# Optimization experiments

Measured on AMD Instinct MI355X. Metric: run time of the kernel, lower is better.

## Reference

```python
import jax, jax.numpy as jnp
import numpy as np

B, C, D = 8192, 5994, 192
M, S = 0.2, 30.0
S_NEG = 1.0
COS_M = float(np.cos(M)); SIN_M = float(np.sin(M))
TH = float(np.cos(M))
MM = float(np.sin(np.pi - M) * M)


def _normalize(v):
    # torch F.normalize: v / max(||v||, eps)
    return v / jnp.maximum(jnp.linalg.norm(v, axis=-1, keepdims=True), 1e-12)


def _ce_label_smooth(logits, targets, eps=0.1):
    # torch CrossEntropyLoss(label_smoothing=eps): target dist = (1-eps)*onehot + eps/C
    logp = jax.nn.log_softmax(logits, axis=-1)
    nll = -jnp.take_along_axis(logp, targets[:, None], axis=-1)[:, 0]
    smooth = -logp.mean(axis=-1)
    return ((1.0 - eps) * nll + eps * smooth).mean()


def setup_inputs() -> dict:
    key = jax.random.key(0)
    kx, kw, kl = jax.random.split(key, 3)
    x = jax.random.normal(kx, (B, D), dtype=jnp.float32)
    std = float(np.sqrt(2.0 / (C + D)))  # xavier_normal_ gain=1
    weight = jax.random.normal(kw, (C, D), dtype=jnp.float32) * std
    # guarantee every class appears so n_unique == C (static shapes)
    extra = jax.random.randint(kl, (B - C,), 0, C, dtype=jnp.int32)
    label = jnp.concatenate([jnp.arange(C, dtype=jnp.int32), extra])
    return {"x": x, "weight": weight, "label": label}


def reference(x, weight, label):
    x1 = _normalize(x)           # [B, D]; x2 = x1.clone() in torch => identical values
    w = _normalize(weight)       # [C, D]
    cosine = x1 @ w.T            # [B, C]

    # per-unique-label mean (segment mean); labels_center == arange(C)
    counts = jax.ops.segment_sum(jnp.ones((x1.shape[0],), x1.dtype), label, num_segments=C)
    mean_x = jax.ops.segment_sum(x1, label, num_segments=C) / counts[:, None]  # [C, D]
    cosine_center = mean_x @ w.T  # [C, C]

    # ArcFace margin on centers
    sine_c = jnp.sqrt(jnp.clip(1.0 - cosine_center * cosine_center, 0.0, 1.0))
    phi_c = jnp.where(cosine_center - TH > 0,
                      cosine_center - MM,
                      cosine_center * COS_M - sine_c * SIN_M)
    eye = jnp.eye(C, dtype=cosine_center.dtype)  # one_hot_center with labels arange(C)
    output_center = (eye * phi_c + (1.0 - eye) * cosine_center) * S

    # ArcFace margin on samples
    sine = jnp.sqrt(jnp.clip(1.0 - cosine * cosine, 0.0, 1.0))
    phi = jnp.where(cosine - TH > 0, cosine - MM, cosine * COS_M - sine * SIN_M)
    one_hot = jax.nn.one_hot(label, C, dtype=cosine.dtype)
    output_sample = (one_hot * phi + (1.0 - one_hot) * cosine) * S

    aam_sample_loss = 0.5 * _ce_label_smooth(output_sample, label)
    aam_center_loss = 0.5 * _ce_label_smooth(output_center, jnp.arange(C, dtype=jnp.int32))

    # contrastive term over class means of cat(x1, x2) (x2 == x1)
    logit_neg = jnp.concatenate([mean_x, mean_x], axis=1)  # [C, 2D]
    G = logit_neg @ logit_neg.T                            # [C, C]
    offdiag = ~jnp.eye(C, dtype=bool)                      # torch zeroes diag then filters != 0
    neg_inf = jnp.array(-jnp.inf, G.dtype)
    vmax = jnp.max(jnp.where(offdiag, G, neg_inf))
    lse1 = jax.scipy.special.logsumexp(jnp.where(offdiag, S_NEG * G, neg_inf))
    lse2 = jax.scipy.special.logsumexp(jnp.where(offdiag, (2.0 - vmax) * (1.0 - G / vmax), neg_inf))
    logit_neg_loss = jax.nn.softplus(lse1 - lse2 + vmax)

    loss = logit_neg_loss + aam_center_loss + aam_sample_loss
    # full_unique_index == label here (unique labels are 0..C-1 sorted)
    return loss, output_sample, output_center[label]
```

## Files before the change

kernel.cpp:

```cpp
#include <hip/hip_runtime.h>
#include <cstdint>
#include <cstddef>

#define CCLS 5994
#define CPAD 6016
#define BATCH 8192
#define KDIM 192
#define EMAX 16
#define NCB 47
#define NT0 3008
#define NT1 2209
#define NTG 1128
#define MEGA_NT (NT0 + NT1 + NTG)
#define CEF 32

#define S_SC 30.0f
#define COSM 0.9800665778412416f
#define SINM 0.19866933079506122f
#define THC  0.9800665778412416f
#define MMC  0.039733866159012244f

typedef __attribute__((ext_vector_type(8))) short short8;
typedef __attribute__((ext_vector_type(4))) float f32x4;
typedef __attribute__((ext_vector_type(2))) float f32x2;
typedef unsigned short u16;
typedef unsigned int u32;

__device__ __forceinline__ u16 f2bf(float f) {
  u32 u = __float_as_uint(f);
  u32 r = (u + 0x7FFFu + ((u >> 16) & 1u)) >> 16;
  return (u16)r;
}

__device__ __forceinline__ float bf2f(u16 v) { return __uint_as_float(((u32)v) << 16); }

__device__ __forceinline__ float arc_phi(float c) {
  float s2 = fminf(fmaxf(1.0f - c * c, 0.0f), 1.0f);
  float sine = sqrtf(s2);
  return (c - THC > 0.0f) ? (c - MMC) : (c * COSM - sine * SINM);
}

__device__ __forceinline__ float shift_of(float vmax) {
  return (2.0f - vmax) * (1.0f + 2.0f / vmax);
}

__device__ __forceinline__ float wave_sum(float v) {
#pragma unroll
  for (int off = 1; off < 64; off <<= 1) v += __shfl_xor(v, off);
  return v;
}

__device__ __forceinline__ void tri_decode(int g, int& by, int& bx) {
  by = 0;
  while (g >= NCB - by) { g -= NCB - by; ++by; }
  bx = by + g;
}

__global__ void zero_k(f32x4* __restrict__ p, int n4) {
  const int i = blockIdx.x * 256 + threadIdx.x;
  if (i < n4) p[i] = (f32x4){0.f, 0.f, 0.f, 0.f};
}

__global__ void norm_w_k(const float* __restrict__ w, u16* __restrict__ wb) {
  const int row = blockIdx.x * 4 + (threadIdx.x >> 6);
  const int lane = threadIdx.x & 63;
  float v0 = 0.f, v1 = 0.f, v2 = 0.f;
  if (row < CCLS) {
    const float* p = w + (size_t)row * KDIM;
    v0 = p[lane]; v1 = p[lane + 64]; v2 = p[lane + 128];
  }
  float ss = wave_sum(v0 * v0 + v1 * v1 + v2 * v2);
  float inv = 1.0f / fmaxf(sqrtf(ss), 1e-12f);
  if (row >= CCLS) inv = 0.f;
  u16* q = wb + (size_t)row * KDIM;
  q[lane] = f2bf(v0 * inv);
  q[lane + 64] = f2bf(v1 * inv);
  q[lane + 128] = f2bf(v2 * inv);
}

__global__ void norm_x_k(const float* __restrict__ x, const int* __restrict__ label,
                         u16* __restrict__ xb, int* __restrict__ ecnt, int* __restrict__ eidx,
                         int* __restrict__ dcnt, int* __restrict__ didx) {
  const int row = blockIdx.x * 4 + (threadIdx.x >> 6);
  const int lane = threadIdx.x & 63;
  const float* p = x + (size_t)row * KDIM;
  float v0 = p[lane], v1 = p[lane + 64], v2 = p[lane + 128];
  float ss = wave_sum(v0 * v0 + v1 * v1 + v2 * v2);
  float inv = 1.0f / fmaxf(sqrtf(ss), 1e-12f);
  u16* q = xb + (size_t)row * KDIM;
  q[lane] = f2bf(v0 * inv); q[lane + 64] = f2bf(v1 * inv); q[lane + 128] = f2bf(v2 * inv);
  if (lane == 0) {
    const int lab = label[row];
    int pos = atomicAdd(&ecnt[lab], 1);
    if (pos < EMAX) eidx[lab * EMAX + pos] = row;
    if (row >= CCLS) {
      int dp = atomicAdd(&dcnt[lab], 1);
      if (dp < EMAX) didx[lab * EMAX + dp] = row;
    }
  }
}

__global__ void mean_k(const u16* __restrict__ xb, const int* __restrict__ ecnt,
                       const int* __restrict__ eidx, u16* __restrict__ mb) {
  const int row = blockIdx.x * 4 + (threadIdx.x >> 6);
  const int lane = threadIdx.x & 63;
  u16* q = mb + (size_t)row * KDIM;
  if (row < CCLS) {
    const int n = min(ecnt[row], EMAX);
    float s0 = 0.f, s1 = 0.f, s2 = 0.f;
    for (int j = 0; j < n; ++j) {
      const u16* p = xb + (size_t)eidx[row * EMAX + j] * KDIM;
      s0 += bf2f(p[lane]); s1 += bf2f(p[lane + 64]); s2 += bf2f(p[lane + 128]);
    }
    const float inv = 1.0f / (float)n;
    q[lane] = f2bf(s0 * inv); q[lane + 64] = f2bf(s1 * inv); q[lane + 128] = f2bf(s2 * inv);
  } else {
    q[lane] = 0; q[lane + 64] = 0; q[lane + 128] = 0;
  }
}

__device__ __forceinline__ void stage64(const u16* __restrict__ A, const u16* __restrict__ Bm,
                                        int row0, int col0, int wid, int lane, int k0,
                                        u16* As, u16* Bs) {
  const int sw = (((lane & 7) ^ ((lane >> 3) & 7))) * 8;
#pragma unroll
  for (int i = 0; i < 4; ++i) {
    const int c = wid * 4 + i;
    const int r = c * 8 + (lane >> 3);
    const u16* ga = A + (size_t)(row0 + r) * KDIM + (k0 + sw);
    const u16* gb = Bm + (size_t)(col0 + r) * KDIM + (k0 + sw);
    __builtin_amdgcn_global_load_lds((const __attribute__((address_space(1))) void*)ga,
                                     (__attribute__((address_space(3))) void*)(As + c * 512),
                                     16, 0, 0);
    __builtin_amdgcn_global_load_lds((const __attribute__((address_space(1))) void*)gb,
                                     (__attribute__((address_space(3))) void*)(Bs + c * 512),
                                     16, 0, 0);
  }
}

__device__ __forceinline__ void gemm_core(const u16* __restrict__ A, const u16* __restrict__ Bm,
                                          int row0, int col0, int wid, int lane,
                                          int wm, int wn, u16 (*lds)[8192], f32x4 (&acc)[4][4]) {
#pragma unroll
  for (int i = 0; i < 4; ++i)
#pragma unroll
    for (int j = 0; j < 4; ++j)
      acc[i][j] = (f32x4){0.f, 0.f, 0.f, 0.f};
  for (int k0 = 0; k0 < KDIM; k0 += 64) {
    stage64(A, Bm, row0, col0, wid, lane, k0, &lds[0][0], &lds[1][0]);
    asm volatile("s_waitcnt vmcnt(0)" ::: "memory");
    __syncthreads();
#pragma unroll
    for (int kk = 0; kk < 2; ++kk) {
      short8 af[4], bf[4];
#pragma unroll
      for (int mi = 0; mi < 4; ++mi) {
        const int R = wm * 64 + mi * 16 + (lane & 15);
        const int sl = ((kk * 4 + (lane >> 4)) ^ (lane & 7)) * 8;
        af[mi] = *(const short8*)&lds[0][R * 64 + sl];
      }
#pragma unroll
      for (int ni = 0; ni < 4; ++ni) {
        const int R = wn * 64 + ni * 16 + (lane & 15);
        const int sl = ((kk * 4 + (lane >> 4)) ^ (lane & 7)) * 8;
        bf[ni] = *(const short8*)&lds[1][R * 64 + sl];
      }
#pragma unroll
      for (int mi = 0; mi < 4; ++mi)
#pragma unroll
        for (int ni = 0; ni < 4; ++ni)
          acc[mi][ni] = __builtin_amdgcn_mfma_f32_16x16x32_bf16(af[mi], bf[ni], acc[mi][ni], 0, 0, 0);
    }
    __syncthreads();
  }
}

__device__ __forceinline__ void epi_af(f32x4 (&acc)[4][4], float* __restrict__ out,
                                       const int* __restrict__ label, int is_center, int plane,
                                       int row0, int col0, int bx, int tid, int lane, int wid,
                                       int wm, int wn, u16 (*lds)[8192],
                                       float* __restrict__ pse, float* __restrict__ psm,
                                       float* __restrict__ rowtgt,
                                       const int* __restrict__ dcnt, const int* __restrict__ didx) {
  float* sred = (float*)&lds[0][0];
  const int rl = (lane >> 4) * 4;
  const int cl = lane & 15;
#pragma unroll
  for (int mi = 0; mi < 4; ++mi) {
#pragma unroll
    for (int r = 0; r < 4; ++r) {
      const int gr = row0 + wm * 64 + mi * 16 + rl + r;
      const int valid_r = !is_center || gr < CCLS;
      const int tgt = is_center ? gr : label[gr];
      float se = 0.f, sm = 0.f;
#pragma unroll
      for (int ni = 0; ni < 4; ++ni) {
        const int gc = col0 + wn * 64 + ni * 16 + cl;
        float v = acc[mi][ni][r];
        float val = ((gc == tgt) ? arc_phi(v) : v) * S_SC;
        acc[mi][ni][r] = val;
        if (gc < CCLS && valid_r) {
          se += __expf(val - 30.0f);
          sm += val;
          if (gc == tgt) rowtgt[gr] = val;
        }
      }
#pragma unroll
      for (int m = 1; m < 16; m <<= 1) {
        se += __shfl_xor(se, m);
        sm += __shfl_xor(sm, m);
      }
      if (cl == 0) {
        const int lr = wm * 64 + mi * 16 + rl + r;
        sred[lr * 2 + wn] = se;
        sred[256 + lr * 2 + wn] = sm;
      }
    }
  }
  __syncthreads();
  if (tid < 128) {
    const int gr = row0 + tid;
    if (!is_center || gr < CCLS) {
      float se = sred[tid * 2] + sred[tid * 2 + 1];
      float sm = sred[256 + tid * 2] + sred[256 + tid * 2 + 1];
      pse[(size_t)bx * plane + gr] = se;
      psm[(size_t)bx * plane + gr] = sm;
    }
  }
  float* sC = (float*)&lds[0][0];
#pragma unroll
  for (int half = 0; half < 2; ++half) {
    __syncthreads();
    if (wm == half) {
#pragma unroll
      for (int mi = 0; mi < 4; ++mi)
#pragma unroll
        for (int ni = 0; ni < 4; ++ni)
#pragma unroll
          for (int r = 0; r < 4; ++r)
            sC[(mi * 16 + rl + r) * 128 + wn * 64 + ni * 16 + cl] = acc[mi][ni][r];
    }
    __syncthreads();
#pragma unroll
    for (int i = 0; i < 16; ++i) {
      const int lr = wid * 16 + i;
      const int gr = row0 + half * 64 + lr;
      if (is_center && gr >= CCLS) continue;
      const int gc = col0 + lane * 2;
      if (gc < CCLS) {
        f32x2 v = *(const f32x2*)&sC[lr * 128 + lane * 2];
        __builtin_nontemporal_store(v, (f32x2*)(out + (size_t)gr * CCLS + gc));
      }
    }
    if (is_center) {
      for (int i = 0; i < 16; ++i) {
        const int lr = wid * 16 + i;
        const int gr = row0 + half * 64 + lr;
        if (gr >= CCLS) continue;
        const int n = min(dcnt[gr], EMAX);
        for (int j = 0; j < n; ++j) {
          const int b = didx[gr * EMAX + j];
          const int gc = col0 + lane * 2;
          if (gc < CCLS) {
            f32x2 v = *(const f32x2*)&sC[lr * 128 + lane * 2];
            __builtin_nontemporal_store(v, (f32x2*)(out + (size_t)b * CCLS + gc));
          }
        }
      }
    }
  }
}

__device__ __forceinline__ void epi_gram(f32x4 (&acc)[4][4], float* __restrict__ scal, int pass2,
                                         float aco, float cco, int row0, int col0, int diag,
                                         int tid, int lane, int wid, int wm, int wn,
                                         u16 (*lds)[8192]) {
  float* sred = (float*)&lds[0][0];
  const int rl = (lane >> 4) * 4;
  const int cl = lane & 15;
  float lsum = 0.f;
  float lmax = -3.0e38f;
#pragma unroll
  for (int mi = 0; mi < 4; ++mi)
#pragma unroll
    for (int r = 0; r < 4; ++r) {
      const int gi = row0 + wm * 64 + mi * 16 + rl + r;
#pragma unroll
      for (int ni = 0; ni < 4; ++ni) {
        const int gj = col0 + wn * 64 + ni * 16 + cl;
        if (gi < CCLS && gj < CCLS && gi != gj) {
          float g = 2.0f * acc[mi][ni][r];
          if (!pass2) {
            lsum += __expf(g - 2.0f);
            lmax = fmaxf(lmax, g);
          } else {
            lsum += __expf(fmaf(aco, g, cco));
          }
        }
      }
    }
  const float wgt = diag ? 1.0f : 2.0f;
  lsum = wave_sum(lsum) * wgt;
  if (!pass2) {
#pragma unroll
    for (int off = 1; off < 64; off <<= 1) lmax = fmaxf(lmax, __shfl_xor(lmax, off));
  }
  __syncthreads();
  if (lane == 0) { sred[wid] = lsum; sred[4 + wid] = lmax; }
  __syncthreads();
  if (tid == 0) {
    float s = sred[0] + sred[1] + sred[2] + sred[3];
    atomicAdd(&scal[pass2 ? 2 : 1], s);
    if (!pass2) {
      float m = fmaxf(fmaxf(sred[4], sred[5]), fmaxf(sred[6], sred[7]));
      u32 b = __float_as_uint(m);
      u32 enc = (b & 0x80000000u) ? ~b : (b | 0x80000000u);
      atomicMax((u32*)&scal[0], enc);
    }
  }
}

__launch_bounds__(256)
__global__ void mega_k(const u16* __restrict__ xb, const u16* __restrict__ wb,
                       const u16* __restrict__ mb, const int* __restrict__ label,
                       float* __restrict__ out1, float* __restrict__ out2,
                       float* __restrict__ scal,
                       float* __restrict__ pse_s, float* __restrict__ psm_s,
                       float* __restrict__ rowtgt_s,
                       float* __restrict__ pse_c, float* __restrict__ psm_c,
                       float* __restrict__ rowtgt_c,
                       const int* __restrict__ dcnt, const int* __restrict__ didx) {
  __shared__ u16 lds[2][8192];
  const int tid = threadIdx.x;
  const int lane = tid & 63;
  const int wid = tid >> 6;
  const int wm = wid >> 1, wn = wid & 1;
  const int t = blockIdx.x;

  f32x4 acc[4][4];
  if (t < NT0) {
    const int bx = t % NCB, by = t / NCB;
    gemm_core(xb, wb, by * 128, bx * 128, wid, lane, wm, wn, lds, acc);
    epi_af(acc, out1, label, 0, BATCH, by * 128, bx * 128, bx, tid, lane, wid, wm, wn,
           lds, pse_s, psm_s, rowtgt_s, nullptr, nullptr);
  } else if (t < NT0 + NT1) {
    const int u = t - NT0;
    const int bx = u % NCB, by = u / NCB;
    gemm_core(mb, wb, by * 128, bx * 128, wid, lane, wm, wn, lds, acc);
    epi_af(acc, out2, label, 1, CPAD, by * 128, bx * 128, bx, tid, lane, wid, wm, wn,
           lds, pse_c, psm_c, rowtgt_c, dcnt, didx);
  } else {
    int by, bx;
    tri_decode(t - NT0 - NT1, by, bx);
    gemm_core(mb, mb, by * 128, bx * 128, wid, lane, wm, wn, lds, acc);
    epi_gram(acc, scal, 0, 0.f, 0.f, by * 128, bx * 128, bx == by, tid, lane, wid, wm, wn, lds);
  }
}

__launch_bounds__(256)
__global__ void fin2_k(const u16* __restrict__ mb, float* __restrict__ scal,
                       const float* __restrict__ pse_s, const float* __restrict__ psm_s,
                       const float* __restrict__ rowtgt_s,
                       const float* __restrict__ pse_c, const float* __restrict__ psm_c,
                       const float* __restrict__ rowtgt_c) {
  __shared__ u16 lds[2][8192];
  const int tid = threadIdx.x;
  const int lane = tid & 63;
  const int wid = tid >> 6;
  const int wm = wid >> 1, wn = wid & 1;
  const int t = blockIdx.x;

  if (t < NTG) {
    u32 u = __float_as_uint(scal[0]);
    u32 bits = (u & 0x80000000u) ? (u ^ 0x80000000u) : ~u;
    const float vmax = __uint_as_float(bits);
    const float aco = -(2.0f - vmax) / vmax;
    const float cco = (2.0f - vmax) - shift_of(vmax);
    int by, bx;
    tri_decode(t, by, bx);
    f32x4 acc[4][4];
    gemm_core(mb, mb, by * 128, bx * 128, wid, lane, wm, wn, lds, acc);
    epi_gram(acc, scal, 1, aco, cco, by * 128, bx * 128, bx == by, tid, lane, wid, wm, wn, lds);
  } else {
    const int i = (t - NTG) * 256 + tid;
    float ls = 0.f, lc = 0.f;
    if (i < BATCH) {
      float se = 0.f, sm = 0.f;
#pragma unroll 1
      for (int p = 0; p < NCB; ++p) { se += pse_s[p * BATCH + i]; sm += psm_s[p * BATCH + i]; }
      ls = 30.0f + logf(se) - 0.9f * rowtgt_s[i] - (0.1f / (float)CCLS) * sm;
    }
    if (i < CCLS) {
      float se = 0.f, sm = 0.f;
#pragma unroll 1
      for (int p = 0; p < NCB; ++p) { se += pse_c[p * CPAD + i]; sm += psm_c[p * CPAD + i]; }
      lc = 30.0f + logf(se) - 0.9f * rowtgt_c[i] - (0.1f / (float)CCLS) * sm;
    }
    ls = wave_sum(ls);
    lc = wave_sum(lc);
    if (lane == 0) {
      atomicAdd(&scal[3], ls);
      atomicAdd(&scal[4], lc);
    }
  }
}

__global__ void finalize_k(const float* __restrict__ scal, float* __restrict__ out) {
  u32 u = __float_as_uint(scal[0]);
  u32 bits = (u & 0x80000000u) ? (u ^ 0x80000000u) : ~u;
  float vmax = __uint_as_float(bits);
  float s1 = scal[1], s2 = scal[2], ces = scal[3], cec = scal[4];
  float lse1 = 2.0f + logf(s1);
  float lse2 = shift_of(vmax) + logf(s2);
  float z = lse1 - lse2 + vmax;
  float sp = (z > 20.f) ? z : log1pf(expf(z));
  out[0] = sp + 0.5f * (cec / (float)CCLS) + 0.5f * (ces / (float)BATCH);
}

extern "C" void kernel_launch(void* const* d_in, const int* in_sizes, int n_in,
                              void* d_out, int out_size, void* d_ws, size_t ws_size,
                              hipStream_t stream) {
  (void)in_sizes; (void)n_in; (void)out_size; (void)ws_size;
  const float* x = (const float*)d_in[0];
  const float* w = (const float*)d_in[1];
  const int* label = (const int*)d_in[2];
  float* out = (float*)d_out;
  float* out1 = out + 1;
  float* out2 = out + 1 + (size_t)BATCH * CCLS;

  char* ws = (char*)d_ws;
  size_t o = 0;
  u16* xb = (u16*)(ws + o); o += (size_t)BATCH * KDIM * 2;
  u16* wb = (u16*)(ws + o); o += (size_t)CPAD * KDIM * 2;
  u16* mb = (u16*)(ws + o); o += (size_t)CPAD * KDIM * 2;
  const size_t zo = o;
  float* scal = (float*)(ws + o); o += 256;
  int* ecnt = (int*)(ws + o); o += (size_t)CPAD * 4;
  int* dcnt = (int*)(ws + o); o += (size_t)CPAD * 4;
  const size_t ze = o;
  int* eidx = (int*)(ws + o); o += (size_t)CPAD * EMAX * 4;
  int* didx = (int*)(ws + o); o += (size_t)CPAD * EMAX * 4;
  float* rowtgt_s = (float*)(ws + o); o += (size_t)BATCH * 4;
  float* rowtgt_c = (float*)(ws + o); o += (size_t)CPAD * 4;
  float* pse_s = (float*)(ws + o); o += (size_t)NCB * BATCH * 4;
  float* psm_s = (float*)(ws + o); o += (size_t)NCB * BATCH * 4;
  float* pse_c = (float*)(ws + o); o += (size_t)NCB * CPAD * 4;
  float* psm_c = (float*)(ws + o); o += (size_t)NCB * CPAD * 4;

  const int n4 = (int)((ze - zo) / 16);
  zero_k<<<(n4 + 255) / 256, 256, 0, stream>>>((f32x4*)(ws + zo), n4);

  norm_w_k<<<CPAD / 4, 256, 0, stream>>>(w, wb);
  norm_x_k<<<BATCH / 4, 256, 0, stream>>>(x, label, xb, ecnt, eidx, dcnt, didx);
  mean_k<<<CPAD / 4, 256, 0, stream>>>(xb, ecnt, eidx, mb);

  mega_k<<<MEGA_NT, 256, 0, stream>>>(xb, wb, mb, label, out1, out2, scal,
                                      pse_s, psm_s, rowtgt_s, pse_c, psm_c, rowtgt_c,
                                      dcnt, didx);
  fin2_k<<<NTG + CEF, 256, 0, stream>>>(mb, scal, pse_s, psm_s, rowtgt_s,
                                        pse_c, psm_c, rowtgt_c);

  finalize_k<<<1, 1, 0, stream>>>(scal, out);
}
```

Measured before the change: 291.3 us.

## Replace tiled GEMM-epilogue with per-row-strip blocks that finish CE loss in-block

The 128x128 tiled sample/center GEMM blocks are replaced by 444 strip blocks. Each block owns 32 rows and loops over all 47 column tiles, loading operands straight from global memory without LDS staging. Row-wise softmax sums and the target logit are kept in LDS across the column loop, so each block computes its cross-entropy contribution directly. This removes the per-tile partial-sum buffers and the separate reduction blocks in the second kernel. The trade-off is far fewer blocks, which may underfill the GPU and serialize the large output writes, plus repeated global loads of the weight tile per strip.

```diff
diff --git a/kernel.cpp b/kernel.cpp
--- a/kernel.cpp
+++ b/kernel.cpp
@@ -8,11 +8,11 @@
 #define KDIM 192
 #define EMAX 16
 #define NCB 47
-#define NT0 3008
-#define NT1 2209
+#define NSS 256
+#define NSC 188
+#define NSTRIP (NSS + NSC)
 #define NTG 1128
-#define MEGA_NT (NT0 + NT1 + NTG)
-#define CEF 32
+#define MEGA_NT (NSTRIP + NTG)
 
 #define S_SC 30.0f
 #define COSM 0.9800665778412416f
@@ -175,102 +175,6 @@
   }
 }
 
-__device__ __forceinline__ void epi_af(f32x4 (&acc)[4][4], float* __restrict__ out,
-                                       const int* __restrict__ label, int is_center, int plane,
-                                       int row0, int col0, int bx, int tid, int lane, int wid,
-                                       int wm, int wn, u16 (*lds)[8192],
-                                       float* __restrict__ pse, float* __restrict__ psm,
-                                       float* __restrict__ rowtgt,
-                                       const int* __restrict__ dcnt, const int* __restrict__ didx) {
-  float* sred = (float*)&lds[0][0];
-  const int rl = (lane >> 4) * 4;
-  const int cl = lane & 15;
-#pragma unroll
-  for (int mi = 0; mi < 4; ++mi) {
-#pragma unroll
-    for (int r = 0; r < 4; ++r) {
-      const int gr = row0 + wm * 64 + mi * 16 + rl + r;
-      const int valid_r = !is_center || gr < CCLS;
-      const int tgt = is_center ? gr : label[gr];
-      float se = 0.f, sm = 0.f;
-#pragma unroll
-      for (int ni = 0; ni < 4; ++ni) {
-        const int gc = col0 + wn * 64 + ni * 16 + cl;
-        float v = acc[mi][ni][r];
-        float val = ((gc == tgt) ? arc_phi(v) : v) * S_SC;
-        acc[mi][ni][r] = val;
-        if (gc < CCLS && valid_r) {
-          se += __expf(val - 30.0f);
-          sm += val;
-          if (gc == tgt) rowtgt[gr] = val;
-        }
-      }
-#pragma unroll
-      for (int m = 1; m < 16; m <<= 1) {
-        se += __shfl_xor(se, m);
-        sm += __shfl_xor(sm, m);
-      }
-      if (cl == 0) {
-        const int lr = wm * 64 + mi * 16 + rl + r;
-        sred[lr * 2 + wn] = se;
-        sred[256 + lr * 2 + wn] = sm;
-      }
-    }
-  }
-  __syncthreads();
-  if (tid < 128) {
-    const int gr = row0 + tid;
-    if (!is_center || gr < CCLS) {
-      float se = sred[tid * 2] + sred[tid * 2 + 1];
-      float sm = sred[256 + tid * 2] + sred[256 + tid * 2 + 1];
-      pse[(size_t)bx * plane + gr] = se;
-      psm[(size_t)bx * plane + gr] = sm;
-    }
-  }
-  float* sC = (float*)&lds[0][0];
-#pragma unroll
-  for (int half = 0; half < 2; ++half) {
-    __syncthreads();
-    if (wm == half) {
-#pragma unroll
-      for (int mi = 0; mi < 4; ++mi)
-#pragma unroll
-        for (int ni = 0; ni < 4; ++ni)
-#pragma unroll
-          for (int r = 0; r < 4; ++r)
-            sC[(mi * 16 + rl + r) * 128 + wn * 64 + ni * 16 + cl] = acc[mi][ni][r];
-    }
-    __syncthreads();
-#pragma unroll
-    for (int i = 0; i < 16; ++i) {
-      const int lr = wid * 16 + i;
-      const int gr = row0 + half * 64 + lr;
-      if (is_center && gr >= CCLS) continue;
-      const int gc = col0 + lane * 2;
-      if (gc < CCLS) {
-        f32x2 v = *(const f32x2*)&sC[lr * 128 + lane * 2];
-        __builtin_nontemporal_store(v, (f32x2*)(out + (size_t)gr * CCLS + gc));
-      }
-    }
-    if (is_center) {
-      for (int i = 0; i < 16; ++i) {
-        const int lr = wid * 16 + i;
-        const int gr = row0 + half * 64 + lr;
-        if (gr >= CCLS) continue;
-        const int n = min(dcnt[gr], EMAX);
-        for (int j = 0; j < n; ++j) {
-          const int b = didx[gr * EMAX + j];
-          const int gc = col0 + lane * 2;
-          if (gc < CCLS) {
-            f32x2 v = *(const f32x2*)&sC[lr * 128 + lane * 2];
-            __builtin_nontemporal_store(v, (f32x2*)(out + (size_t)b * CCLS + gc));
-          }
-        }
-      }
-    }
-  }
-}
-
 __device__ __forceinline__ void epi_gram(f32x4 (&acc)[4][4], float* __restrict__ scal, int pass2,
                                          float aco, float cco, int row0, int col0, int diag,
                                          int tid, int lane, int wid, int wm, int wn,
@@ -325,84 +229,171 @@
                        const u16* __restrict__ mb, const int* __restrict__ label,
                        float* __restrict__ out1, float* __restrict__ out2,
                        float* __restrict__ scal,
-                       float* __restrict__ pse_s, float* __restrict__ psm_s,
-                       float* __restrict__ rowtgt_s,
-                       float* __restrict__ pse_c, float* __restrict__ psm_c,
-                       float* __restrict__ rowtgt_c,
                        const int* __restrict__ dcnt, const int* __restrict__ didx) {
+  __shared__ char smem[32768];
+  const int tid = threadIdx.x;
+  const int lane = tid & 63;
+  const int w = tid >> 6;
+  const int t = blockIdx.x;
+
+  if (t < NSTRIP) {
+    float* sC = (float*)smem;
+    float* s_se = (float*)(smem + 16384);
+    float* s_sm = (float*)(smem + 16896);
+    float* s_rt = (float*)(smem + 17408);
+    int* s_dc = (int*)(smem + 17536);
+    const int is_center = t >= NSS;
+    const int row0 = (is_center ? t - NSS : t) * 32;
+    const u16* A = is_center ? mb : xb;
+    float* outp = is_center ? out2 : out1;
+    const int cl = lane & 15;
+    const int kq = lane >> 4;
+
+    if (tid < 128) { s_se[tid] = 0.f; s_sm[tid] = 0.f; }
+    if (tid < 32) {
+      s_rt[tid] = 0.f;
+      const int gr = row0 + tid;
+      s_dc[tid] = (is_center && gr < CCLS) ? min(dcnt[gr], EMAX) : 0;
+    }
+    __syncthreads();
+
+    int tg[2][4];
+#pragma unroll
+    for (int mi = 0; mi < 2; ++mi)
+#pragma unroll
+      for (int r = 0; r < 4; ++r) {
+        const int gr = row0 + mi * 16 + kq * 4 + r;
+        tg[mi][r] = is_center ? gr : label[gr];
+      }
+
+    const u16* a0p = A + (size_t)(row0 + cl) * KDIM;
+    const u16* a1p = A + (size_t)(row0 + 16 + cl) * KDIM;
+
+    for (int c = 0; c < NCB; ++c) {
+      const int col0 = c * 128;
+      const u16* b0p = wb + (size_t)(col0 + w * 32 + cl) * KDIM;
+      const u16* b1p = wb + (size_t)(col0 + w * 32 + 16 + cl) * KDIM;
+
+      f32x4 acc[2][2];
+#pragma unroll
+      for (int mi = 0; mi < 2; ++mi)
+#pragma unroll
+        for (int ni = 0; ni < 2; ++ni)
+          acc[mi][ni] = (f32x4){0.f, 0.f, 0.f, 0.f};
+
+#pragma unroll
+      for (int k0 = 0; k0 < KDIM; k0 += 64) {
+#pragma unroll
+        for (int kk = 0; kk < 2; ++kk) {
+          const int ko = k0 + kk * 32 + kq * 8;
+          short8 a0 = *(const short8*)(a0p + ko);
+          short8 a1 = *(const short8*)(a1p + ko);
+          short8 b0 = *(const short8*)(b0p + ko);
+          short8 b1 = *(const short8*)(b1p + ko);
+          acc[0][0] = __builtin_amdgcn_mfma_f32_16x16x32_bf16(a0, b0, acc[0][0], 0, 0, 0);
+          acc[0][1] = __builtin_amdgcn_mfma_f32_16x16x32_bf16(a0, b1, acc[0][1], 0, 0, 0);
+          acc[1][0] = __builtin_amdgcn_mfma_f32_16x16x32_bf16(a1, b0, acc[1][0], 0, 0, 0);
+          acc[1][1] = __builtin_amdgcn_mfma_f32_16x16x32_bf16(a1, b1, acc[1][1], 0, 0, 0);
+        }
+      }
+
+#pragma unroll
+      for (int mi = 0; mi < 2; ++mi) {
+#pragma unroll
+        for (int r = 0; r < 4; ++r) {
+          const int lr = mi * 16 + kq * 4 + r;
+          const int gr = row0 + lr;
+          const int vr = !is_center || gr < CCLS;
+          const int tgt = tg[mi][r];
+          float se = 0.f, sm = 0.f;
+#pragma unroll
+          for (int ni = 0; ni < 2; ++ni) {
+            const int gc = col0 + w * 32 + ni * 16 + cl;
+            float v = acc[mi][ni][r];
+            const bool ist = (gc == tgt);
+            float val = (ist ? arc_phi(v) : v) * S_SC;
+            if (gc < CCLS && vr) {
+              se += __expf(val - 30.0f);
+              sm += val;
+              if (ist) s_rt[lr] = val;
+            }
+            sC[lr * 128 + w * 32 + ni * 16 + cl] = val;
+          }
+#pragma unroll
+          for (int m = 1; m < 16; m <<= 1) {
+            se += __shfl_xor(se, m);
+            sm += __shfl_xor(sm, m);
+          }
+          if (cl == 0) {
+            s_se[w * 32 + lr] += se;
+            s_sm[w * 32 + lr] += sm;
+          }
+        }
+      }
+      asm volatile("s_waitcnt lgkmcnt(0)\ns_barrier" ::: "memory");
+      __builtin_amdgcn_sched_barrier(0);
+#pragma unroll
+      for (int i = 0; i < 8; ++i) {
+        const int lr = w * 8 + i;
+        const int gr = row0 + lr;
+        const int gc = col0 + lane * 2;
+        if ((!is_center || gr < CCLS) && gc + 2 <= CCLS) {
+          f32x2 v = *(const f32x2*)&sC[lr * 128 + lane * 2];
+          __builtin_nontemporal_store(v, (f32x2*)(outp + (size_t)gr * CCLS + gc));
+          const int nd = s_dc[lr];
+          for (int j = 0; j < nd; ++j) {
+            const int b = didx[gr * EMAX + j];
+            __builtin_nontemporal_store(v, (f32x2*)(outp + (size_t)b * CCLS + gc));
+          }
+        }
+      }
+      asm volatile("s_waitcnt lgkmcnt(0)\ns_barrier" ::: "memory");
+      __builtin_amdgcn_sched_barrier(0);
+    }
+
+    __syncthreads();
+    if (tid < 64) {
+      float loss = 0.f;
+      if (tid < 32) {
+        const int gr = row0 + tid;
+        if (!is_center || gr < CCLS) {
+          float set = s_se[tid] + s_se[32 + tid] + s_se[64 + tid] + s_se[96 + tid];
+          float smt = s_sm[tid] + s_sm[32 + tid] + s_sm[64 + tid] + s_sm[96 + tid];
+          loss = 30.0f + logf(set) - 0.9f * s_rt[tid] - (0.1f / (float)CCLS) * smt;
+        }
+      }
+      loss = wave_sum(loss);
+      if (lane == 0) atomicAdd(&scal[is_center ? 4 : 3], loss);
+    }
+  } else {
+    u16 (*lds)[8192] = (u16(*)[8192])smem;
+    const int wm = w >> 1, wn = w & 1;
+    int by, bx;
+    tri_decode(t - NSTRIP, by, bx);
+    f32x4 acc[4][4];
+    gemm_core(mb, mb, by * 128, bx * 128, w, lane, wm, wn, lds, acc);
+    epi_gram(acc, scal, 0, 0.f, 0.f, by * 128, bx * 128, bx == by, tid, lane, w, wm, wn, lds);
+  }
+}
+
+__launch_bounds__(256)
+__global__ void fin2_k(const u16* __restrict__ mb, float* __restrict__ scal) {
   __shared__ u16 lds[2][8192];
   const int tid = threadIdx.x;
   const int lane = tid & 63;
   const int wid = tid >> 6;
   const int wm = wid >> 1, wn = wid & 1;
-  const int t = blockIdx.x;
-
+
+  u32 u = __float_as_uint(scal[0]);
+  u32 bits = (u & 0x80000000u) ? (u ^ 0x80000000u) : ~u;
+  const float vmax = __uint_as_float(bits);
+  const float aco = -(2.0f - vmax) / vmax;
+  const float cco = (2.0f - vmax) - shift_of(vmax);
+  int by, bx;
+  tri_decode(blockIdx.x, by, bx);
   f32x4 acc[4][4];
-  if (t < NT0) {
-    const int bx = t % NCB, by = t / NCB;
-    gemm_core(xb, wb, by * 128, bx * 128, wid, lane, wm, wn, lds, acc);
-    epi_af(acc, out1, label, 0, BATCH, by * 128, bx * 128, bx, tid, lane, wid, wm, wn,
-           lds, pse_s, psm_s, rowtgt_s, nullptr, nullptr);
-  } else if (t < NT0 + NT1) {
-    const int u = t - NT0;
-    const int bx = u % NCB, by = u / NCB;
-    gemm_core(mb, wb, by * 128, bx * 128, wid, lane, wm, wn, lds, acc);
-    epi_af(acc, out2, label, 1, CPAD, by * 128, bx * 128, bx, tid, lane, wid, wm, wn,
-           lds, pse_c, psm_c, rowtgt_c, dcnt, didx);
-  } else {
-    int by, bx;
-    tri_decode(t - NT0 - NT1, by, bx);
-    gemm_core(mb, mb, by * 128, bx * 128, wid, lane, wm, wn, lds, acc);
-    epi_gram(acc, scal, 0, 0.f, 0.f, by * 128, bx * 128, bx == by, tid, lane, wid, wm, wn, lds);
-  }
-}
-
-__launch_bounds__(256)
-__global__ void fin2_k(const u16* __restrict__ mb, float* __restrict__ scal,
-                       const float* __restrict__ pse_s, const float* __restrict__ psm_s,
-                       const float* __restrict__ rowtgt_s,
-                       const float* __restrict__ pse_c, const float* __restrict__ psm_c,
-                       const float* __restrict__ rowtgt_c) {
-  __shared__ u16 lds[2][8192];
-  const int tid = threadIdx.x;
-  const int lane = tid & 63;
-  const int wid = tid >> 6;
-  const int wm = wid >> 1, wn = wid & 1;
-  const int t = blockIdx.x;
-
-  if (t < NTG) {
-    u32 u = __float_as_uint(scal[0]);
-    u32 bits = (u & 0x80000000u) ? (u ^ 0x80000000u) : ~u;
-    const float vmax = __uint_as_float(bits);
-    const float aco = -(2.0f - vmax) / vmax;
-    const float cco = (2.0f - vmax) - shift_of(vmax);
-    int by, bx;
-    tri_decode(t, by, bx);
-    f32x4 acc[4][4];
-    gemm_core(mb, mb, by * 128, bx * 128, wid, lane, wm, wn, lds, acc);
-    epi_gram(acc, scal, 1, aco, cco, by * 128, bx * 128, bx == by, tid, lane, wid, wm, wn, lds);
-  } else {
-    const int i = (t - NTG) * 256 + tid;
-    float ls = 0.f, lc = 0.f;
-    if (i < BATCH) {
-      float se = 0.f, sm = 0.f;
-#pragma unroll 1
-      for (int p = 0; p < NCB; ++p) { se += pse_s[p * BATCH + i]; sm += psm_s[p * BATCH + i]; }
-      ls = 30.0f + logf(se) - 0.9f * rowtgt_s[i] - (0.1f / (float)CCLS) * sm;
-    }
-    if (i < CCLS) {
-      float se = 0.f, sm = 0.f;
-#pragma unroll 1
-      for (int p = 0; p < NCB; ++p) { se += pse_c[p * CPAD + i]; sm += psm_c[p * CPAD + i]; }
-      lc = 30.0f + logf(se) - 0.9f * rowtgt_c[i] - (0.1f / (float)CCLS) * sm;
-    }
-    ls = wave_sum(ls);
-    lc = wave_sum(lc);
-    if (lane == 0) {
-      atomicAdd(&scal[3], ls);
-      atomicAdd(&scal[4], lc);
-    }
-  }
+  gemm_core(mb, mb, by * 128, bx * 128, wid, lane, wm, wn, lds, acc);
+  epi_gram(acc, scal, 1, aco, cco, by * 128, bx * 128, bx == by, tid, lane, wid, wm, wn, lds);
 }
 
 __global__ void finalize_k(const float* __restrict__ scal, float* __restrict__ out) {
@@ -440,12 +431,6 @@
   const size_t ze = o;
   int* eidx = (int*)(ws + o); o += (size_t)CPAD * EMAX * 4;
   int* didx = (int*)(ws + o); o += (size_t)CPAD * EMAX * 4;
-  float* rowtgt_s = (float*)(ws + o); o += (size_t)BATCH * 4;
-  float* rowtgt_c = (float*)(ws + o); o += (size_t)CPAD * 4;
-  float* pse_s = (float*)(ws + o); o += (size_t)NCB * BATCH * 4;
-  float* psm_s = (float*)(ws + o); o += (size_t)NCB * BATCH * 4;
-  float* pse_c = (float*)(ws + o); o += (size_t)NCB * CPAD * 4;
-  float* psm_c = (float*)(ws + o); o += (size_t)NCB * CPAD * 4;
 
   const int n4 = (int)((ze - zo) / 16);
   zero_k<<<(n4 + 255) / 256, 256, 0, stream>>>((f32x4*)(ws + zo), n4);
@@ -454,11 +439,8 @@
   norm_x_k<<<BATCH / 4, 256, 0, stream>>>(x, label, xb, ecnt, eidx, dcnt, didx);
   mean_k<<<CPAD / 4, 256, 0, stream>>>(xb, ecnt, eidx, mb);
 
-  mega_k<<<MEGA_NT, 256, 0, stream>>>(xb, wb, mb, label, out1, out2, scal,
-                                      pse_s, psm_s, rowtgt_s, pse_c, psm_c, rowtgt_c,
-                                      dcnt, didx);
-  fin2_k<<<NTG + CEF, 256, 0, stream>>>(mb, scal, pse_s, psm_s, rowtgt_s,
-                                        pse_c, psm_c, rowtgt_c);
+  mega_k<<<MEGA_NT, 256, 0, stream>>>(xb, wb, mb, label, out1, out2, scal, dcnt, didx);
+  fin2_k<<<NTG, 256, 0, stream>>>(mb, scal);
 
   finalize_k<<<1, 1, 0, stream>>>(scal, out);
 }
```

New measurement: 430.3 us. 1.48x slower.

## Load MFMA operands directly from global memory instead of staging through LDS

Applied to the files above, without the earlier changes.

Replaces the LDS-staged GEMM main loop (global_load_lds plus barriers per 64-wide K chunk) with a direct-to-register load of short8 fragments from global memory for each of six K steps. This removes the syncthreads and LDS round trips in the K loop, since K is only 192. In exchange, operands shared between the two waves of a row or column are no longer reused through LDS, so each wave fetches them from global or L2 itself. Access is also strided across rows, which may raise global traffic and latency exposure. The shared buffer is retyped as a single float array used only by the epilogues.

```diff
diff --git a/kernel.cpp b/kernel.cpp
--- a/kernel.cpp
+++ b/kernel.cpp
@@ -119,70 +119,43 @@
   }
 }
 
-__device__ __forceinline__ void stage64(const u16* __restrict__ A, const u16* __restrict__ Bm,
-                                        int row0, int col0, int wid, int lane, int k0,
-                                        u16* As, u16* Bs) {
-  const int sw = (((lane & 7) ^ ((lane >> 3) & 7))) * 8;
-#pragma unroll
-  for (int i = 0; i < 4; ++i) {
-    const int c = wid * 4 + i;
-    const int r = c * 8 + (lane >> 3);
-    const u16* ga = A + (size_t)(row0 + r) * KDIM + (k0 + sw);
-    const u16* gb = Bm + (size_t)(col0 + r) * KDIM + (k0 + sw);
-    __builtin_amdgcn_global_load_lds((const __attribute__((address_space(1))) void*)ga,
-                                     (__attribute__((address_space(3))) void*)(As + c * 512),
-                                     16, 0, 0);
-    __builtin_amdgcn_global_load_lds((const __attribute__((address_space(1))) void*)gb,
-                                     (__attribute__((address_space(3))) void*)(Bs + c * 512),
-                                     16, 0, 0);
-  }
-}
-
-__device__ __forceinline__ void gemm_core(const u16* __restrict__ A, const u16* __restrict__ Bm,
-                                          int row0, int col0, int wid, int lane,
-                                          int wm, int wn, u16 (*lds)[8192], f32x4 (&acc)[4][4]) {
+__device__ __forceinline__ void gemm_direct(const u16* __restrict__ A, const u16* __restrict__ Bm,
+                                            int row0, int col0, int wm, int wn, int lane,
+                                            f32x4 (&acc)[4][4]) {
+  const int cl = lane & 15;
+  const int kq = lane >> 4;
 #pragma unroll
   for (int i = 0; i < 4; ++i)
 #pragma unroll
     for (int j = 0; j < 4; ++j)
       acc[i][j] = (f32x4){0.f, 0.f, 0.f, 0.f};
-  for (int k0 = 0; k0 < KDIM; k0 += 64) {
-    stage64(A, Bm, row0, col0, wid, lane, k0, &lds[0][0], &lds[1][0]);
-    asm volatile("s_waitcnt vmcnt(0)" ::: "memory");
-    __syncthreads();
-#pragma unroll
-    for (int kk = 0; kk < 2; ++kk) {
-      short8 af[4], bf[4];
-#pragma unroll
-      for (int mi = 0; mi < 4; ++mi) {
-        const int R = wm * 64 + mi * 16 + (lane & 15);
-        const int sl = ((kk * 4 + (lane >> 4)) ^ (lane & 7)) * 8;
-        af[mi] = *(const short8*)&lds[0][R * 64 + sl];
-      }
-#pragma unroll
-      for (int ni = 0; ni < 4; ++ni) {
-        const int R = wn * 64 + ni * 16 + (lane & 15);
-        const int sl = ((kk * 4 + (lane >> 4)) ^ (lane & 7)) * 8;
-        bf[ni] = *(const short8*)&lds[1][R * 64 + sl];
-      }
-#pragma unroll
-      for (int mi = 0; mi < 4; ++mi)
-#pragma unroll
-        for (int ni = 0; ni < 4; ++ni)
-          acc[mi][ni] = __builtin_amdgcn_mfma_f32_16x16x32_bf16(af[mi], bf[ni], acc[mi][ni], 0, 0, 0);
-    }
-    __syncthreads();
+  const u16* ap = A + (size_t)(row0 + wm * 64 + cl) * KDIM + kq * 8;
+  const u16* bp = Bm + (size_t)(col0 + wn * 64 + cl) * KDIM + kq * 8;
+#pragma unroll
+  for (int t = 0; t < 6; ++t) {
+    short8 af[4], bf[4];
+#pragma unroll
+    for (int mi = 0; mi < 4; ++mi)
+      af[mi] = *(const short8*)(ap + (size_t)mi * 16 * KDIM + t * 32);
+#pragma unroll
+    for (int ni = 0; ni < 4; ++ni)
+      bf[ni] = *(const short8*)(bp + (size_t)ni * 16 * KDIM + t * 32);
+#pragma unroll
+    for (int mi = 0; mi < 4; ++mi)
+#pragma unroll
+      for (int ni = 0; ni < 4; ++ni)
+        acc[mi][ni] = __builtin_amdgcn_mfma_f32_16x16x32_bf16(af[mi], bf[ni], acc[mi][ni], 0, 0, 0);
   }
 }
 
 __device__ __forceinline__ void epi_af(f32x4 (&acc)[4][4], float* __restrict__ out,
                                        const int* __restrict__ label, int is_center, int plane,
                                        int row0, int col0, int bx, int tid, int lane, int wid,
-                                       int wm, int wn, u16 (*lds)[8192],
+                                       int wm, int wn, float* __restrict__ smem,
                                        float* __restrict__ pse, float* __restrict__ psm,
                                        float* __restrict__ rowtgt,
                                        const int* __restrict__ dcnt, const int* __restrict__ didx) {
-  float* sred = (float*)&lds[0][0];
+  float* sred = smem;
   const int rl = (lane >> 4) * 4;
   const int cl = lane & 15;
 #pragma unroll
@@ -227,7 +200,7 @@
       psm[(size_t)bx * plane + gr] = sm;
     }
   }
-  float* sC = (float*)&lds[0][0];
+  float* sC = smem;
 #pragma unroll
   for (int half = 0; half < 2; ++half) {
     __syncthreads();
@@ -274,8 +247,8 @@
 __device__ __forceinline__ void epi_gram(f32x4 (&acc)[4][4], float* __restrict__ scal, int pass2,
                                          float aco, float cco, int row0, int col0, int diag,
                                          int tid, int lane, int wid, int wm, int wn,
-                                         u16 (*lds)[8192]) {
-  float* sred = (float*)&lds[0][0];
+                                         float* __restrict__ smem) {
+  float* sred = smem;
   const int rl = (lane >> 4) * 4;
   const int cl = lane & 15;
   float lsum = 0.f;
@@ -330,7 +303,7 @@
                        float* __restrict__ pse_c, float* __restrict__ psm_c,
                        float* __restrict__ rowtgt_c,
                        const int* __restrict__ dcnt, const int* __restrict__ didx) {
-  __shared__ u16 lds[2][8192];
+  __shared__ float smem[8192];
   const int tid = threadIdx.x;
   const int lane = tid & 63;
   const int wid = tid >> 6;
@@ -340,20 +313,20 @@
   f32x4 acc[4][4];
   if (t < NT0) {
     const int bx = t % NCB, by = t / NCB;
-    gemm_core(xb, wb, by * 128, bx * 128, wid, lane, wm, wn, lds, acc);
+    gemm_direct(xb, wb, by * 128, bx * 128, wm, wn, lane, acc);
     epi_af(acc, out1, label, 0, BATCH, by * 128, bx * 128, bx, tid, lane, wid, wm, wn,
-           lds, pse_s, psm_s, rowtgt_s, nullptr, nullptr);
+           smem, pse_s, psm_s, rowtgt_s, nullptr, nullptr);
   } else if (t < NT0 + NT1) {
     const int u = t - NT0;
     const int bx = u % NCB, by = u / NCB;
-    gemm_core(mb, wb, by * 128, bx * 128, wid, lane, wm, wn, lds, acc);
+    gemm_direct(mb, wb, by * 128, bx * 128, wm, wn, lane, acc);
     epi_af(acc, out2, label, 1, CPAD, by * 128, bx * 128, bx, tid, lane, wid, wm, wn,
-           lds, pse_c, psm_c, rowtgt_c, dcnt, didx);
+           smem, pse_c, psm_c, rowtgt_c, dcnt, didx);
   } else {
     int by, bx;
     tri_decode(t - NT0 - NT1, by, bx);
-    gemm_core(mb, mb, by * 128, bx * 128, wid, lane, wm, wn, lds, acc);
-    epi_gram(acc, scal, 0, 0.f, 0.f, by * 128, bx * 128, bx == by, tid, lane, wid, wm, wn, lds);
+    gemm_direct(mb, mb, by * 128, bx * 128, wm, wn, lane, acc);
+    epi_gram(acc, scal, 0, 0.f, 0.f, by * 128, bx * 128, bx == by, tid, lane, wid, wm, wn, smem);
   }
 }
 
@@ -363,7 +336,7 @@
                        const float* __restrict__ rowtgt_s,
                        const float* __restrict__ pse_c, const float* __restrict__ psm_c,
                        const float* __restrict__ rowtgt_c) {
-  __shared__ u16 lds[2][8192];
+  __shared__ float smem[8192];
   const int tid = threadIdx.x;
   const int lane = tid & 63;
   const int wid = tid >> 6;
@@ -379,8 +352,8 @@
     int by, bx;
     tri_decode(t, by, bx);
     f32x4 acc[4][4];
-    gemm_core(mb, mb, by * 128, bx * 128, wid, lane, wm, wn, lds, acc);
-    epi_gram(acc, scal, 1, aco, cco, by * 128, bx * 128, bx == by, tid, lane, wid, wm, wn, lds);
+    gemm_direct(mb, mb, by * 128, bx * 128, wm, wn, lane, acc);
+    epi_gram(acc, scal, 1, aco, cco, by * 128, bx * 128, bx == by, tid, lane, wid, wm, wn, smem);
   } else {
     const int i = (t - NTG) * 256 + tid;
     float ls = 0.f, lc = 0.f;
```

New measurement: 348.3 us. +19.6%, slower.

## Replace second Gram GEMM pass with histogram-based logsumexp approximation

Applied to the files above, without the earlier changes.

Instead of recomputing the class-mean Gram matrix in a second pass once vmax is known, the first pass bins every off-diagonal Gram value into a 1024-bin histogram using LDS atomics merged into a global histogram. The finalize kernel then evaluates the second logsumexp from bin centers. This removes a full extra GEMM over the upper-triangular tiles. In exchange it adds shared-memory atomic contention and introduces a quantization error in the contrastive loss term.

```diff
diff --git a/kernel.cpp b/kernel.cpp
--- a/kernel.cpp
+++ b/kernel.cpp
@@ -13,6 +13,7 @@
 #define NTG 1128
 #define MEGA_NT (NT0 + NT1 + NTG)
 #define CEF 32
+#define NBINS 1024
 
 #define S_SC 30.0f
 #define COSM 0.9800665778412416f
@@ -38,10 +39,6 @@
   float s2 = fminf(fmaxf(1.0f - c * c, 0.0f), 1.0f);
   float sine = sqrtf(s2);
   return (c - THC > 0.0f) ? (c - MMC) : (c * COSM - sine * SINM);
-}
-
-__device__ __forceinline__ float shift_of(float vmax) {
-  return (2.0f - vmax) * (1.0f + 2.0f / vmax);
 }
 
 __device__ __forceinline__ float wave_sum(float v) {
@@ -271,13 +268,16 @@
   }
 }
 
-__device__ __forceinline__ void epi_gram(f32x4 (&acc)[4][4], float* __restrict__ scal, int pass2,
-                                         float aco, float cco, int row0, int col0, int diag,
+__device__ __forceinline__ void epi_gram(f32x4 (&acc)[4][4], float* __restrict__ scal,
+                                         u32* __restrict__ ghist,
+                                         int row0, int col0, int diag,
                                          int tid, int lane, int wid, int wm, int wn,
                                          u16 (*lds)[8192]) {
   float* sred = (float*)&lds[0][0];
+  u32* histl = (u32*)(sred + 64);
   const int rl = (lane >> 4) * 4;
   const int cl = lane & 15;
+  const u32 wgt = diag ? 1u : 2u;
   float lsum = 0.f;
   float lmax = -3.0e38f;
 #pragma unroll
@@ -290,33 +290,48 @@
         const int gj = col0 + wn * 64 + ni * 16 + cl;
         if (gi < CCLS && gj < CCLS && gi != gj) {
           float g = 2.0f * acc[mi][ni][r];
-          if (!pass2) {
-            lsum += __expf(g - 2.0f);
-            lmax = fmaxf(lmax, g);
-          } else {
-            lsum += __expf(fmaf(aco, g, cco));
-          }
+          lsum += __expf(g - 2.0f);
+          lmax = fmaxf(lmax, g);
         }
       }
     }
-  const float wgt = diag ? 1.0f : 2.0f;
-  lsum = wave_sum(lsum) * wgt;
-  if (!pass2) {
-#pragma unroll
-    for (int off = 1; off < 64; off <<= 1) lmax = fmaxf(lmax, __shfl_xor(lmax, off));
-  }
+  lsum = wave_sum(lsum) * (float)wgt;
+#pragma unroll
+  for (int off = 1; off < 64; off <<= 1) lmax = fmaxf(lmax, __shfl_xor(lmax, off));
+
   __syncthreads();
+  for (int i = tid; i < NBINS; i += 256) histl[i] = 0;
   if (lane == 0) { sred[wid] = lsum; sred[4 + wid] = lmax; }
   __syncthreads();
+
+#pragma unroll
+  for (int mi = 0; mi < 4; ++mi)
+#pragma unroll
+    for (int r = 0; r < 4; ++r) {
+      const int gi = row0 + wm * 64 + mi * 16 + rl + r;
+#pragma unroll
+      for (int ni = 0; ni < 4; ++ni) {
+        const int gj = col0 + wn * 64 + ni * 16 + cl;
+        if (gi < CCLS && gj < CCLS && gi != gj) {
+          float g = 2.0f * acc[mi][ni][r];
+          int idx = (int)((g + 2.0f) * 256.0f);
+          idx = min(NBINS - 1, max(0, idx));
+          atomicAdd(&histl[idx], wgt);
+        }
+      }
+    }
   if (tid == 0) {
     float s = sred[0] + sred[1] + sred[2] + sred[3];
-    atomicAdd(&scal[pass2 ? 2 : 1], s);
-    if (!pass2) {
-      float m = fmaxf(fmaxf(sred[4], sred[5]), fmaxf(sred[6], sred[7]));
-      u32 b = __float_as_uint(m);
-      u32 enc = (b & 0x80000000u) ? ~b : (b | 0x80000000u);
-      atomicMax((u32*)&scal[0], enc);
-    }
+    atomicAdd(&scal[1], s);
+    float m = fmaxf(fmaxf(sred[4], sred[5]), fmaxf(sred[6], sred[7]));
+    u32 b = __float_as_uint(m);
+    u32 enc = (b & 0x80000000u) ? ~b : (b | 0x80000000u);
+    atomicMax((u32*)&scal[0], enc);
+  }
+  __syncthreads();
+  for (int i = tid; i < NBINS; i += 256) {
+    const u32 n = histl[i];
+    if (n) atomicAdd(&ghist[i], n);
   }
 }
 
@@ -324,7 +339,7 @@
 __global__ void mega_k(const u16* __restrict__ xb, const u16* __restrict__ wb,
                        const u16* __restrict__ mb, const int* __restrict__ label,
                        float* __restrict__ out1, float* __restrict__ out2,
-                       float* __restrict__ scal,
+                       float* __restrict__ scal, u32* __restrict__ ghist,
                        float* __restrict__ pse_s, float* __restrict__ psm_s,
                        float* __restrict__ rowtgt_s,
                        float* __restrict__ pse_c, float* __restrict__ psm_c,
@@ -353,68 +368,63 @@
     int by, bx;
     tri_decode(t - NT0 - NT1, by, bx);
     gemm_core(mb, mb, by * 128, bx * 128, wid, lane, wm, wn, lds, acc);
-    epi_gram(acc, scal, 0, 0.f, 0.f, by * 128, bx * 128, bx == by, tid, lane, wid, wm, wn, lds);
+    epi_gram(acc, scal, ghist, by * 128, bx * 128, bx == by, tid, lane, wid, wm, wn, lds);
   }
 }
 
 __launch_bounds__(256)
-__global__ void fin2_k(const u16* __restrict__ mb, float* __restrict__ scal,
-                       const float* __restrict__ pse_s, const float* __restrict__ psm_s,
-                       const float* __restrict__ rowtgt_s,
-                       const float* __restrict__ pse_c, const float* __restrict__ psm_c,
-                       const float* __restrict__ rowtgt_c) {
-  __shared__ u16 lds[2][8192];
+__global__ void ce_fin_k(float* __restrict__ scal,
+                         const float* __restrict__ pse_s, const float* __restrict__ psm_s,
+                         const float* __restrict__ rowtgt_s,
+                         const float* __restrict__ pse_c, const float* __restrict__ psm_c,
+                         const float* __restrict__ rowtgt_c) {
+  const int i = blockIdx.x * 256 + threadIdx.x;
+  float ls = 0.f, lc = 0.f;
+  if (i < BATCH) {
+    float se = 0.f, sm = 0.f;
+#pragma unroll 1
+    for (int p = 0; p < NCB; ++p) { se += pse_s[p * BATCH + i]; sm += psm_s[p * BATCH + i]; }
+    ls = 30.0f + logf(se) - 0.9f * rowtgt_s[i] - (0.1f / (float)CCLS) * sm;
+  }
+  if (i < CCLS) {
+    float se = 0.f, sm = 0.f;
+#pragma unroll 1
+    for (int p = 0; p < NCB; ++p) { se += pse_c[p * CPAD + i]; sm += psm_c[p * CPAD + i]; }
+    lc = 30.0f + logf(se) - 0.9f * rowtgt_c[i] - (0.1f / (float)CCLS) * sm;
+  }
+  ls = wave_sum(ls);
+  lc = wave_sum(lc);
+  if ((threadIdx.x & 63) == 0) {
+    atomicAdd(&scal[3], ls);
+    atomicAdd(&scal[4], lc);
+  }
+}
+
+__global__ void finalize_k(const float* __restrict__ scal, const u32* __restrict__ ghist,
+                           float* __restrict__ out) {
+  __shared__ float red[4];
   const int tid = threadIdx.x;
-  const int lane = tid & 63;
-  const int wid = tid >> 6;
-  const int wm = wid >> 1, wn = wid & 1;
-  const int t = blockIdx.x;
-
-  if (t < NTG) {
-    u32 u = __float_as_uint(scal[0]);
-    u32 bits = (u & 0x80000000u) ? (u ^ 0x80000000u) : ~u;
-    const float vmax = __uint_as_float(bits);
-    const float aco = -(2.0f - vmax) / vmax;
-    const float cco = (2.0f - vmax) - shift_of(vmax);
-    int by, bx;
-    tri_decode(t, by, bx);
-    f32x4 acc[4][4];
-    gemm_core(mb, mb, by * 128, bx * 128, wid, lane, wm, wn, lds, acc);
-    epi_gram(acc, scal, 1, aco, cco, by * 128, bx * 128, bx == by, tid, lane, wid, wm, wn, lds);
-  } else {
-    const int i = (t - NTG) * 256 + tid;
-    float ls = 0.f, lc = 0.f;
-    if (i < BATCH) {
-      float se = 0.f, sm = 0.f;
-#pragma unroll 1
-      for (int p = 0; p < NCB; ++p) { se += pse_s[p * BATCH + i]; sm += psm_s[p * BATCH + i]; }
-      ls = 30.0f + logf(se) - 0.9f * rowtgt_s[i] - (0.1f / (float)CCLS) * sm;
-    }
-    if (i < CCLS) {
-      float se = 0.f, sm = 0.f;
-#pragma unroll 1
-      for (int p = 0; p < NCB; ++p) { se += pse_c[p * CPAD + i]; sm += psm_c[p * CPAD + i]; }
-      lc = 30.0f + logf(se) - 0.9f * rowtgt_c[i] - (0.1f / (float)CCLS) * sm;
-    }
-    ls = wave_sum(ls);
-    lc = wave_sum(lc);
-    if (lane == 0) {
-      atomicAdd(&scal[3], ls);
-      atomicAdd(&scal[4], lc);
-    }
-  }
-}
-
-__global__ void finalize_k(const float* __restrict__ scal, float* __restrict__ out) {
   u32 u = __float_as_uint(scal[0]);
   u32 bits = (u & 0x80000000u) ? (u ^ 0x80000000u) : ~u;
-  float vmax = __uint_as_float(bits);
-  float s1 = scal[1], s2 = scal[2], ces = scal[3], cec = scal[4];
-  float lse1 = 2.0f + logf(s1);
-  float lse2 = shift_of(vmax) + logf(s2);
-  float z = lse1 - lse2 + vmax;
-  float sp = (z > 20.f) ? z : log1pf(expf(z));
-  out[0] = sp + 0.5f * (cec / (float)CCLS) + 0.5f * (ces / (float)BATCH);
+  const float vmax = __uint_as_float(bits);
+  const float a = -(2.0f - vmax) / vmax;
+  const float c = (2.0f - vmax);
+  float s = 0.f;
+  for (int b = tid; b < NBINS; b += 256) {
+    const u32 n = ghist[b];
+    if (n) s += (float)n * __expf(a * (-2.0f + ((float)b + 0.5f) * (1.0f / 256.0f)));
+  }
+  s = wave_sum(s);
+  if ((tid & 63) == 0) red[tid >> 6] = s;
+  __syncthreads();
+  if (tid == 0) {
+    const float tot = red[0] + red[1] + red[2] + red[3];
+    const float lse1 = 2.0f + logf(scal[1]);
+    const float lse2 = c + logf(tot);
+    const float z = lse1 - lse2 + vmax;
+    const float sp = (z > 20.f) ? z : log1pf(expf(z));
+    out[0] = sp + 0.5f * (scal[4] / (float)CCLS) + 0.5f * (scal[3] / (float)BATCH);
+  }
 }
 
 extern "C" void kernel_launch(void* const* d_in, const int* in_sizes, int n_in,
@@ -435,6 +445,7 @@
   u16* mb = (u16*)(ws + o); o += (size_t)CPAD * KDIM * 2;
   const size_t zo = o;
   float* scal = (float*)(ws + o); o += 256;
+  u32* ghist = (u32*)(ws + o); o += NBINS * 4;
   int* ecnt = (int*)(ws + o); o += (size_t)CPAD * 4;
   int* dcnt = (int*)(ws + o); o += (size_t)CPAD * 4;
   const size_t ze = o;
@@ -454,11 +465,10 @@
   norm_x_k<<<BATCH / 4, 256, 0, stream>>>(x, label, xb, ecnt, eidx, dcnt, didx);
   mean_k<<<CPAD / 4, 256, 0, stream>>>(xb, ecnt, eidx, mb);
 
-  mega_k<<<MEGA_NT, 256, 0, stream>>>(xb, wb, mb, label, out1, out2, scal,
+  mega_k<<<MEGA_NT, 256, 0, stream>>>(xb, wb, mb, label, out1, out2, scal, ghist,
                                       pse_s, psm_s, rowtgt_s, pse_c, psm_c, rowtgt_c,
                                       dcnt, didx);
-  fin2_k<<<NTG + CEF, 256, 0, stream>>>(mb, scal, pse_s, psm_s, rowtgt_s,
-                                        pse_c, psm_c, rowtgt_c);
-
-  finalize_k<<<1, 1, 0, stream>>>(scal, out);
-}
+  ce_fin_k<<<CEF, 256, 0, stream>>>(scal, pse_s, psm_s, rowtgt_s, pse_c, psm_c, rowtgt_c);
+
+  finalize_k<<<1, 256, 0, stream>>>(scal, ghist, out);
+}
```

Measured after the change: 277.2 us. 1.05x faster.
